# Optimization experiments

Hardware: AMD Instinct MI355X
Metric: run time of the kernel (lower is better)

## Reference

```python
import jax, jax.numpy as jnp
import numpy as np

B, S, H = 2, 2048, 2048
NK, NV, DK, DV = 16, 32, 128, 128
K_CONV = 4
EPS = 1e-6
KEY_DIM = NK * DK          # 2048
VALUE_DIM = NV * DV        # 4096
CONV_DIM = 2 * KEY_DIM + VALUE_DIM  # 8192
R = NV // NK               # GQA repeat factor


def setup_inputs() -> dict:
    key = jax.random.key(0)
    ks = jax.random.split(key, 9)
    s = lambda d: 1.0 / np.sqrt(d)
    x = jax.random.normal(ks[0], (B, S, H), jnp.float32)
    W_qkvz = jax.random.normal(ks[1], (H, 2 * KEY_DIM + 2 * VALUE_DIM), jnp.float32) * s(H)
    W_ba = jax.random.normal(ks[2], (H, 2 * NV), jnp.float32) * s(H)
    conv_w = jax.random.normal(ks[3], (CONV_DIM, K_CONV), jnp.float32) * s(K_CONV)
    dt_bias = jnp.ones((NV,), jnp.float32)
    A_log = jnp.log(jax.random.uniform(ks[4], (NV,), jnp.float32, 1e-3, 16.0))
    norm_w = jnp.ones((DV,), jnp.float32)
    W_out = jax.random.normal(ks[5], (VALUE_DIM, H), jnp.float32) * s(VALUE_DIM)
    return {"x": x, "W_qkvz": W_qkvz, "W_ba": W_ba, "conv_w": conv_w,
            "dt_bias": dt_bias, "A_log": A_log, "norm_w": norm_w, "W_out": W_out}


def _rms_norm(x, eps=EPS):
    return x * jax.lax.rsqrt(jnp.mean(jnp.square(x), -1, keepdims=True) + eps)


def _forward(x, W_qkvz, W_ba, conv_w, dt_bias, A_log, norm_w, W_out):
    b_, s_ = x.shape[:2]
    # in projections (mlx split-INDEX semantics)
    qkvz = (x @ W_qkvz).reshape(b_, s_, NK, 2 * DK + 2 * R * DV)
    q, k, v, z = jnp.split(qkvz, [DK, 2 * DK, 2 * DK + R * DV], axis=-1)
    v = v.reshape(b_, s_, NV, DV)
    z = z.reshape(b_, s_, NV, DV)
    ba = (x @ W_ba).reshape(b_, s_, NK, 2 * R)
    b_gate, a_gate = jnp.split(ba, [R], axis=-1)
    b_gate = b_gate.reshape(b_, s_, NV)
    a_gate = a_gate.reshape(b_, s_, NV)

    # causal depthwise conv over [q,k,v] channels, zero initial conv state
    mixed = jnp.concatenate([q.reshape(b_, s_, -1), k.reshape(b_, s_, -1),
                             v.reshape(b_, s_, -1)], axis=-1)  # [B,S,CONV_DIM]
    xc = jnp.pad(mixed, ((0, 0), (K_CONV - 1, 0), (0, 0))).transpose(0, 2, 1)  # [B,C,S+K-1]
    conv = jax.lax.conv_general_dilated(
        xc, conv_w[:, None, :], window_strides=(1,), padding='VALID',
        dimension_numbers=('NCH', 'OIH', 'NCH'), feature_group_count=CONV_DIM)
    conv = jax.nn.silu(conv).transpose(0, 2, 1)  # [B,S,CONV_DIM]
    q, k, v = jnp.split(conv, [KEY_DIM, 2 * KEY_DIM], axis=-1)
    q = q.reshape(b_, s_, NK, DK)
    k = k.reshape(b_, s_, NK, DK)
    v = v.reshape(b_, s_, NV, DV)

    inv_scale = DK ** -0.5
    q = (inv_scale ** 2) * _rms_norm(q)
    k = inv_scale * _rms_norm(k)
    # GQA: repeat k/q heads to match value heads
    q = jnp.repeat(q, R, axis=2)  # [B,S,NV,DK]
    k = jnp.repeat(k, R, axis=2)

    beta = jax.nn.sigmoid(b_gate)                                # [B,S,NV]
    g = -jnp.exp(A_log) * jax.nn.softplus(a_gate + dt_bias)      # [B,S,NV] (log-decay)

    # gated delta-rule recurrence, scan over time
    def step(Sst, inp):
        q_t, k_t, v_t, g_t, beta_t = inp   # [B,NV,DK], [B,NV,DV], [B,NV]
        Sst = Sst * jnp.exp(g_t)[..., None, None]
        kv = jnp.einsum('bhk,bhkv->bhv', k_t, Sst)
        delta = (v_t - kv) * beta_t[..., None]
        Sst = Sst + k_t[..., None] * delta[:, :, None, :]
        o = jnp.einsum('bhk,bhkv->bhv', q_t, Sst)
        return Sst, o

    S0 = jnp.zeros((b_, NV, DK, DV), x.dtype)
    xs = (q.transpose(1, 0, 2, 3), k.transpose(1, 0, 2, 3), v.transpose(1, 0, 2, 3),
          g.transpose(1, 0, 2), beta.transpose(1, 0, 2))
    _, out = jax.lax.scan(step, S0, xs)
    out = out.transpose(1, 0, 2, 3)  # [B,S,NV,DV]

    # gated RMSNorm (precise swiglu)
    xn = _rms_norm(out) * norm_w
    gated = jax.nn.silu(z.astype(jnp.float32)) * xn.astype(jnp.float32)
    gated = gated.astype(x.dtype)
    return gated.reshape(b_, s_, VALUE_DIM) @ W_out


def reference(x, W_qkvz, W_ba, conv_w, dt_bias, A_log, norm_w, W_out):
    return _forward(x, W_qkvz, W_ba, conv_w, dt_bias, A_log, norm_w, W_out)
```

## Files before the change

### kernel.cpp

```cpp
#include <hip/hip_runtime.h>
#include <stdint.h>

#define B_    2
#define SEQ   2048
#define HID   2048
#define NK_   16
#define NV_   32
#define DK_   128
#define DV_   128
#define NQKVZ 12288
#define CONVD 8192
#define MTOT  (B_*SEQ)
#define CCH   16
#define T0TOK 1264
#define HTOK2 784
#define CT    8
#define RLDSZ 110592

typedef unsigned short ushort_t;
typedef __bf16 bf16x8 __attribute__((ext_vector_type(8)));
typedef float  f32x4  __attribute__((ext_vector_type(4)));
typedef unsigned short us4 __attribute__((ext_vector_type(4)));

__device__ __forceinline__ ushort_t f2bf(float f){
  union { float f; unsigned u; } v; v.f = f;
  unsigned r = v.u + 0x7FFFu + ((v.u >> 16) & 1u);
  return (ushort_t)(r >> 16);
}
__device__ __forceinline__ float bf2f(ushort_t u){
  union { unsigned u; float f; } v; v.u = ((unsigned)u) << 16; return v.f;
}
__device__ __forceinline__ float sigmoidf_(float x){ return 1.f/(1.f+__expf(-x)); }
__device__ __forceinline__ float siluf_(float x){ return x*sigmoidf_(x); }

__global__ void cast_x_kernel(const float* __restrict__ x, ushort_t* __restrict__ xb, int n4){
  int i = blockIdx.x*256 + threadIdx.x;
  if (i >= n4) return;
  float4 v = ((const float4*)x)[i];
  us4 o; o[0]=f2bf(v.x); o[1]=f2bf(v.y); o[2]=f2bf(v.z); o[3]=f2bf(v.w);
  ((us4*)xb)[i] = o;
}

__global__ __launch_bounds__(256) void transpose_cast(const float* __restrict__ W, ushort_t* __restrict__ Wt,
                                                      int K, int N){
  __shared__ float tile[64][65];
  int n0 = blockIdx.x*64, k0 = blockIdx.y*64;
  int tx = threadIdx.x & 63, ty = threadIdx.x >> 6;
  #pragma unroll
  for (int i=0;i<16;i++){
    int kr = ty + i*4;
    tile[kr][tx] = W[(size_t)(k0+kr)*N + n0+tx];
  }
  __syncthreads();
  #pragma unroll
  for (int i=0;i<16;i++){
    int nr = ty + i*4;
    Wt[(size_t)(n0+nr)*K + k0+tx] = f2bf(tile[tx][nr]);
  }
}

template<int OUTBF>
__global__ __launch_bounds__(512, 2) void gemm_big(const ushort_t* __restrict__ A, const ushort_t* __restrict__ Bt,
                                                   void* __restrict__ Cv, int M, int N, int K){
  extern __shared__ ushort_t dynlds[];
  ushort_t* SA = dynlds;
  ushort_t* SB = dynlds + 3*8192;
  const int t = threadIdx.x;
  const int lane = t & 63, w = t >> 6;
  const int wm = w >> 2, wn = w & 3;
  const int lr = lane & 15, hk = lane >> 4;
  const int gx = gridDim.x;
  const int nwg = gx * gridDim.y;
  const int flat = blockIdx.y*gx + blockIdx.x;
  const int cpx = nwg >> 3;
  const int swzb = (flat & 7)*cpx + (flat >> 3);
  const int m0 = (swzb / gx) * 256, n0 = (swzb % gx) * 256;

  int srow[2], scol[2];
  #pragma unroll
  for (int q=0;q<2;q++){
    int p  = (w*2+q)*1024 + lane*16;
    int lg = p ^ (((p>>9)&1)<<5);
    srow[q] = lg >> 6;
    scol[q] = (lg & 63) >> 1;
  }
  int phA[8], phB[4];
  #pragma unroll
  for (int mi=0;mi<8;mi++){
    int lg = (wm*128 + mi*16 + lr)*64 + hk*16;
    phA[mi] = lg ^ (((lg>>9)&1)<<5);
  }
  #pragma unroll
  for (int ni=0;ni<4;ni++){
    int lg = (wn*64 + ni*16 + lr)*64 + hk*16;
    phB[ni] = lg ^ (((lg>>9)&1)<<5);
  }

  auto stage = [&](int j, int bufb){
    #pragma unroll
    for (int q=0;q<2;q++)
      __builtin_amdgcn_global_load_lds(
        (const __attribute__((address_space(1))) void*)(A + (size_t)(m0+srow[q])*K + j*32 + scol[q]),
        (__attribute__((address_space(3))) void*)(SA + bufb*8192 + (w*2+q)*512), 16, 0, 0);
    #pragma unroll
    for (int q=0;q<2;q++)
      __builtin_amdgcn_global_load_lds(
        (const __attribute__((address_space(1))) void*)(Bt + (size_t)(n0+srow[q])*K + j*32 + scol[q]),
        (__attribute__((address_space(3))) void*)(SB + bufb*8192 + (w*2+q)*512), 16, 0, 0);
  };

  f32x4 acc[8][4];
  #pragma unroll
  for (int mi=0;mi<8;mi++)
    #pragma unroll
    for (int ni=0;ni<4;ni++) acc[mi][ni] = (f32x4){0.f,0.f,0.f,0.f};

  const int NT = K >> 5;
  stage(0, 0);
  stage(1, 1);
  asm volatile("s_waitcnt vmcnt(4)" ::: "memory");
  __builtin_amdgcn_s_barrier();
  __builtin_amdgcn_sched_barrier(0);

  int cur = 0;
  for (int j = 0; j < NT; ++j){
    int nb = cur + 2; if (nb >= 3) nb -= 3;
    if (j + 2 < NT) stage(j+2, nb);
    const char* bA = (const char*)(SA + cur*8192);
    const char* bB = (const char*)(SB + cur*8192);
    bf16x8 af[8], bfv[4];
    #pragma unroll
    for (int mi=0;mi<8;mi++) af[mi]  = *(const bf16x8*)(bA + phA[mi]);
    #pragma unroll
    for (int ni=0;ni<4;ni++) bfv[ni] = *(const bf16x8*)(bB + phB[ni]);
    #pragma unroll
    for (int mi=0;mi<8;mi++)
      #pragma unroll
      for (int ni=0;ni<4;ni++)
        acc[mi][ni] = __builtin_amdgcn_mfma_f32_16x16x32_bf16(af[mi], bfv[ni], acc[mi][ni], 0, 0, 0);
    if (j + 2 < NT){
      asm volatile("s_waitcnt vmcnt(4)" ::: "memory");
      __builtin_amdgcn_s_barrier();
      __builtin_amdgcn_sched_barrier(0);
    } else if (j + 1 < NT){
      asm volatile("s_waitcnt vmcnt(0)" ::: "memory");
      __builtin_amdgcn_s_barrier();
      __builtin_amdgcn_sched_barrier(0);
    }
    cur = cur + 1; if (cur >= 3) cur -= 3;
  }

  #pragma unroll
  for (int mi=0;mi<8;mi++)
    #pragma unroll
    for (int ni=0;ni<4;ni++)
      #pragma unroll
      for (int r=0;r<4;r++){
        int m = m0 + wm*128 + mi*16 + hk*4 + r;
        int n = n0 + wn*64  + ni*16 + lr;
        if (OUTBF) ((ushort_t*)Cv)[(size_t)m*N + n] = f2bf(acc[mi][ni][r]);
        else       ((float*)Cv)[(size_t)m*N + n]    = acc[mi][ni][r];
      }
}

template<int OUTBF>
__global__ __launch_bounds__(512, 2) void gemm_big2(const ushort_t* __restrict__ A, const ushort_t* __restrict__ Bt,
                                                    void* __restrict__ Cv, int M, int N, int K){
  extern __shared__ ushort_t dynlds[];
  ushort_t* SA = dynlds;
  ushort_t* SB = dynlds + 3*8192;
  const int t = threadIdx.x;
  const int lane = t & 63, w = t >> 6;
  const int wm = w >> 1, wn = w & 1;
  const int lr = lane & 15, hk = lane >> 4;
  const int gx = gridDim.x;
  const int nwg = gx * gridDim.y;
  const int flat = blockIdx.y*gx + blockIdx.x;
  const int cpx = nwg >> 3;
  const int swzb = (flat & 7)*cpx + (flat >> 3);
  const int m0 = (swzb / gx) * 256, n0 = (swzb % gx) * 128;

  int srA[2], scA[2];
  #pragma unroll
  for (int q=0;q<2;q++){
    int p  = (w*2+q)*1024 + lane*16;
    int lg = p ^ (((p>>9)&1)<<5);
    srA[q] = lg >> 6;
    scA[q] = (lg & 63) >> 1;
  }
  int srB, scB;
  {
    int p  = w*1024 + lane*16;
    int lg = p ^ (((p>>9)&1)<<5);
    srB = lg >> 6;
    scB = (lg & 63) >> 1;
  }
  int phA[4], phB[4];
  #pragma unroll
  for (int mi=0;mi<4;mi++){
    int lg = (wm*64 + mi*16 + lr)*64 + hk*16;
    phA[mi] = lg ^ (((lg>>9)&1)<<5);
  }
  #pragma unroll
  for (int ni=0;ni<4;ni++){
    int lg = (wn*64 + ni*16 + lr)*64 + hk*16;
    phB[ni] = lg ^ (((lg>>9)&1)<<5);
  }

  auto stage = [&](int j, int bufb){
    #pragma unroll
    for (int q=0;q<2;q++)
      __builtin_amdgcn_global_load_lds(
        (const __attribute__((address_space(1))) void*)(A + (size_t)(m0+srA[q])*K + j*32 + scA[q]),
        (__attribute__((address_space(3))) void*)(SA + bufb*8192 + (w*2+q)*512), 16, 0, 0);
    __builtin_amdgcn_global_load_lds(
        (const __attribute__((address_space(1))) void*)(Bt + (size_t)(n0+srB)*K + j*32 + scB),
        (__attribute__((address_space(3))) void*)(SB + bufb*4096 + w*512), 16, 0, 0);
  };

  f32x4 acc[4][4];
  #pragma unroll
  for (int mi=0;mi<4;mi++)
    #pragma unroll
    for (int ni=0;ni<4;ni++) acc[mi][ni] = (f32x4){0.f,0.f,0.f,0.f};

  const int NT = K >> 5;
  stage(0, 0);
  stage(1, 1);
  asm volatile("s_waitcnt vmcnt(3)" ::: "memory");
  __builtin_amdgcn_s_barrier();
  __builtin_amdgcn_sched_barrier(0);

  int cur = 0;
  for (int j = 0; j < NT; ++j){
    int nb = cur + 2; if (nb >= 3) nb -= 3;
    if (j + 2 < NT) stage(j+2, nb);
    const char* bA = (const char*)(SA + cur*8192);
    const char* bB = (const char*)(SB + cur*4096);
    bf16x8 af[4], bfv[4];
    #pragma unroll
    for (int mi=0;mi<4;mi++) af[mi]  = *(const bf16x8*)(bA + phA[mi]);
    #pragma unroll
    for (int ni=0;ni<4;ni++) bfv[ni] = *(const bf16x8*)(bB + phB[ni]);
    #pragma unroll
    for (int mi=0;mi<4;mi++)
      #pragma unroll
      for (int ni=0;ni<4;ni++)
        acc[mi][ni] = __builtin_amdgcn_mfma_f32_16x16x32_bf16(af[mi], bfv[ni], acc[mi][ni], 0, 0, 0);
    if (j + 2 < NT){
      asm volatile("s_waitcnt vmcnt(3)" ::: "memory");
      __builtin_amdgcn_s_barrier();
      __builtin_amdgcn_sched_barrier(0);
    } else if (j + 1 < NT){
      asm volatile("s_waitcnt vmcnt(0)" ::: "memory");
      __builtin_amdgcn_s_barrier();
      __builtin_amdgcn_sched_barrier(0);
    }
    cur = cur + 1; if (cur >= 3) cur -= 3;
  }

  #pragma unroll
  for (int mi=0;mi<4;mi++)
    #pragma unroll
    for (int ni=0;ni<4;ni++)
      #pragma unroll
      for (int r=0;r<4;r++){
        int m = m0 + wm*64 + mi*16 + hk*4 + r;
        int n = n0 + wn*64 + ni*16 + lr;
        if (OUTBF) ((ushort_t*)Cv)[(size_t)m*N + n] = f2bf(acc[mi][ni][r]);
        else       ((float*)Cv)[(size_t)m*N + n]    = acc[mi][ni][r];
      }
}

__global__ __launch_bounds__(256) void gemm_ba(const float* __restrict__ x, const float* __restrict__ Wba,
                                               float* __restrict__ ba){
  int lane = threadIdx.x & 63;
  int wid  = threadIdx.x >> 6;
  int row  = blockIdx.x*4 + wid;
  const float* xr = x + (size_t)row*HID;
  float acc = 0.f;
  for (int k=0;k<HID;k+=4){
    float4 xv = *(const float4*)&xr[k];
    acc += xv.x * Wba[(size_t)(k+0)*64 + lane];
    acc += xv.y * Wba[(size_t)(k+1)*64 + lane];
    acc += xv.z * Wba[(size_t)(k+2)*64 + lane];
    acc += xv.w * Wba[(size_t)(k+3)*64 + lane];
  }
  ba[(size_t)row*64 + lane] = acc;
}

__global__ __launch_bounds__(256) void conv_norm_kernel(const ushort_t* __restrict__ qkvz, const float* __restrict__ conv_w,
                                                        ushort_t* __restrict__ qkv){
  const int blk = blockIdx.x;
  const int bt0 = (blk >> 4) * CT;
  const int ts0 = bt0 & (SEQ-1);
  const int gi = (blk & 15)*4 + (threadIdx.x >> 6);
  const int e2 = threadIdx.x & 63;
  const int dk = 2*e2;
  int col;
  if (gi < 16)       col = gi*768 + dk;
  else if (gi < 32)  col = (gi-16)*768 + 128 + dk;
  else { int nv = gi-32; col = (nv>>1)*768 + 256 + (nv&1)*128 + dk; }
  const int c = gi*128 + dk;
  const float4 w0 = *(const float4*)&conv_w[(size_t)c*4];
  const float4 w1 = *(const float4*)&conv_w[(size_t)(c+1)*4];
  ushort2 h0 = (ts0>=1) ? *(const ushort2*)&qkvz[(size_t)(bt0-3)*NQKVZ + col] : make_ushort2(0,0);
  ushort2 h1 = (ts0>=1) ? *(const ushort2*)&qkvz[(size_t)(bt0-2)*NQKVZ + col] : make_ushort2(0,0);
  ushort2 h2 = (ts0>=1) ? *(const ushort2*)&qkvz[(size_t)(bt0-1)*NQKVZ + col] : make_ushort2(0,0);
  const float scale = (gi < 16) ? (1.f/128.f) : 0.08838834764831845f;
  #pragma unroll
  for (int tt=0; tt<CT; ++tt){
    const int bt = bt0 + tt;
    ushort2 h3 = *(const ushort2*)&qkvz[(size_t)bt*NQKVZ + col];
    float y0 = siluf_(bf2f(h0.x)*w0.x + bf2f(h1.x)*w0.y + bf2f(h2.x)*w0.z + bf2f(h3.x)*w0.w);
    float y1 = siluf_(bf2f(h0.y)*w1.x + bf2f(h1.y)*w1.y + bf2f(h2.y)*w1.z + bf2f(h3.y)*w1.w);
    float o0 = y0, o1 = y1;
    if (gi < 32){
      float ss = y0*y0 + y1*y1;
      #pragma unroll
      for (int o=1;o<64;o<<=1) ss += __shfl_xor(ss, o);
      float rs = rsqrtf(ss*(1.f/128.f) + 1e-6f);
      o0 = y0*rs*scale; o1 = y1*rs*scale;
    }
    ushort2 ov; ov.x = f2bf(o0); ov.y = f2bf(o1);
    *(ushort2*)&qkv[(size_t)bt*CONVD + gi*128 + dk] = ov;
    h0 = h1; h1 = h2; h2 = h3;
  }
}

__global__ void gbeta_kernel(const float* __restrict__ ba, const float* __restrict__ A_log,
                             const float* __restrict__ dt_bias, float2* __restrict__ egb){
  int idx = blockIdx.x*256 + threadIdx.x;
  if (idx >= MTOT*NV_) return;
  int nv = idx & 31;
  int bt = idx >> 5;
  int nk = nv >> 1, r = nv & 1;
  float bg = ba[(size_t)bt*64 + nk*4 + r];
  float ag = ba[(size_t)bt*64 + nk*4 + 2 + r];
  float ad = ag + dt_bias[nv];
  float sp = fmaxf(ad, 0.f) + log1pf(__expf(-fabsf(ad)));
  float g  = -__expf(A_log[nv]) * sp;
  egb[idx] = make_float2(g, sigmoidf_(bg));
}

__global__ __launch_bounds__(512) void recurrence_chunked(const ushort_t* __restrict__ qkv,
                                                          const float2* __restrict__ egb,
                                                          float* __restrict__ outc,
                                                          ushort_t* __restrict__ oaug,
                                                          ushort_t* __restrict__ Sfin,
                                                          int pmode){
  extern __shared__ char rlds[];
  ushort_t* Kl  = (ushort_t*)(rlds + 0);
  ushort_t* S0h = (ushort_t*)(rlds + 4352);
  ushort_t* S0l = (ushort_t*)(rlds + 21760);
  ushort_t* T0h = (ushort_t*)(rlds + 39168);
  ushort_t* T0l = (ushort_t*)(rlds + 56576);
  ushort_t* KT  = (ushort_t*)(rlds + 73984);
  ushort_t* DT  = (ushort_t*)(rlds + 84224);
  ushort_t* Wl  = (ushort_t*)(rlds + 94464);
  float*    Al  = (float*)   (rlds + 95744);
  float*    Ul  = (float*)   (rlds + 97024);
  float*    clB = (float*)   (rlds + 107264);
  float*    blB = clB + 32;
  float*    eclB= clB + 64;
  float*    kslB= clB + 96;
  float*    c15B= clB + 128;

  const int bi = blockIdx.x;
  int hb, tokbase, ntok;
  bool ismrg = false, wsf = false;
  if (pmode == 0){ hb = bi; tokbase = 0; ntok = SEQ; }
  else {
    if (bi < 128){ hb = bi; tokbase = 0; ntok = T0TOK; wsf = true; }
    else { hb = bi - 128; tokbase = T0TOK; ntok = HTOK2; ismrg = true; }
  }
  const int b    = hb >> 6;
  const int nv   = (hb >> 1) & 31;
  const int half = hb & 1;
  const int nk   = nv >> 1;
  const int t    = threadIdx.x;
  const int lane = t & 63, w = t >> 6;
  const int lr   = lane & 15, hk = lane >> 4;

  for (int i = t; i < 128*40; i += 512){ KT[i] = 0; DT[i] = 0; }
  for (int i = t; i < 16*40;  i += 512) Wl[i] = 0;
  for (int i = t; i < 64*136; i += 512){
    S0h[i] = 0; S0l[i] = 0;
    if (ismrg){ T0h[i] = 0; T0l[i] = 0; }
  }
  __syncthreads();
  if (ismrg && t < 64) T0h[t*136 + half*64 + t] = (ushort_t)0x3F80;

  const int dt  = w >> 1;
  const int dkb = (w & 1) * 4;
  const int ot  = w - 4;
  const int st  = t >> 5, sdk = (t & 31) * 4;
  const size_t bt0 = (size_t)b*SEQ + tokbase;
  const int mytile = (w < 4) ? w : (w - 4);

  f32x4 S[4], T[4];
  #pragma unroll
  for (int tt=0;tt<4;tt++)
    #pragma unroll
    for (int r=0;r<4;r++){
      S[tt][r] = 0.f;
      T[tt][r] = (ismrg && ((dkb+tt)*16 + hk*4 + r) == (half*64 + dt*16 + lr)) ? 1.f : 0.f;
    }

  uint2 kreg = *(const uint2*)(qkv + (bt0+st)*CONVD + 2048 + nk*128 + sdk);
  bf16x8 qf[4];
  if (w >= 4){
    const ushort_t* qrow = qkv + (bt0+lr)*CONVD + nk*128 + hk*8;
    #pragma unroll
    for (int ks=0;ks<4;ks++) qf[ks] = *(const bf16x8*)(qrow + ks*32);
  }
  ushort_t vreg[4] = {0,0,0,0};
  if (w < 4){
    #pragma unroll
    for (int r=0;r<4;r++)
      vreg[r] = qkv[(bt0+hk*4+r)*CONVD + 4096 + nv*128 + half*64 + w*16 + lr];
  }
  {
    float2 gb = make_float2(0.f,0.f);
    if (w==1 && lane<16) gb = egb[(bt0+lane)*NV_ + nv];
    *(uint2*)&Kl[st*136 + sdk] = kreg;
    if (w==1 && lane<16){
      float c = gb.x;
      #pragma unroll
      for (int o=1;o<16;o<<=1){ float tv = __shfl_up(c, o, 16); if (lane >= o) c += tv; }
      clB[lane] = c; blB[lane] = gb.y; eclB[lane] = __expf(c);
      float c15 = __shfl(c, 15, 16);
      kslB[lane] = __expf(c15 - c);
      if (lane==0) c15B[0] = c15;
    }
  }
  __syncthreads();

  int pb = 0;
  for (int base = 0; base < ntok; base += CCH){
    const int nbase = (base + CCH < ntok) ? base + CCH : base;
    const int pb16 = pb*16;

    bf16x8 kf[4];
    if (w <= 4){
      #pragma unroll
      for (int ks=0;ks<4;ks++) kf[ks] = *(const bf16x8*)&Kl[lr*136 + hk*8 + ks*32];
    }
    f32x4 ph = (f32x4){0.f,0.f,0.f,0.f}, pl = ph, phA = ph, plA = ph;
    __builtin_amdgcn_s_setprio(1);
    #pragma unroll
    for (int ks=0;ks<4;ks++){
      bf16x8 xf = (w < 4) ? kf[ks] : qf[ks];
      bf16x8 yh = *(const bf16x8*)&S0h[(mytile*16+lr)*136 + hk*8 + ks*32];
      bf16x8 yl = *(const bf16x8*)&S0l[(mytile*16+lr)*136 + hk*8 + ks*32];
      ph = __builtin_amdgcn_mfma_f32_16x16x32_bf16(xf, yh, ph, 0,0,0);
      pl = __builtin_amdgcn_mfma_f32_16x16x32_bf16(xf, yl, pl, 0,0,0);
    }
    if (ismrg){
      #pragma unroll
      for (int ks=0;ks<4;ks++){
        bf16x8 xf = (w < 4) ? kf[ks] : qf[ks];
        bf16x8 yh = *(const bf16x8*)&T0h[(mytile*16+lr)*136 + hk*8 + ks*32];
        bf16x8 yl = *(const bf16x8*)&T0l[(mytile*16+lr)*136 + hk*8 + ks*32];
        phA = __builtin_amdgcn_mfma_f32_16x16x32_bf16(xf, yh, phA, 0,0,0);
        plA = __builtin_amdgcn_mfma_f32_16x16x32_bf16(xf, yl, plA, 0,0,0);
      }
    }
    __builtin_amdgcn_s_setprio(0);
    if (w == 1){
      f32x4 a = (f32x4){0.f,0.f,0.f,0.f};
      #pragma unroll
      for (int ks=0;ks<4;ks++) a = __builtin_amdgcn_mfma_f32_16x16x32_bf16(kf[ks], kf[ks], a, 0,0,0);
      #pragma unroll
      for (int r=0;r<4;r++){
        int i = hk*4 + r, j = lr;
        Al[i*20 + j] = (j < i) ? blB[pb16+i]*__expf(clB[pb16+i]-clB[pb16+j])*a[r] : 0.f;
      }
    }
    if (w == 4){
      f32x4 a = (f32x4){0.f,0.f,0.f,0.f};
      #pragma unroll
      for (int ks=0;ks<4;ks++) a = __builtin_amdgcn_mfma_f32_16x16x32_bf16(qf[ks], kf[ks], a, 0,0,0);
      #pragma unroll
      for (int r=0;r<4;r++){
        int i = hk*4 + r, j = lr;
        float val = (j <= i) ? __expf(clB[pb16+i]-clB[pb16+j])*a[r] : 0.f;
        Wl[i*40 + j] = f2bf(val);
      }
    }
    if (w < 4){
      float4 uu;
      #pragma unroll
      for (int r=0;r<4;r++){
        int i = hk*4 + r;
        ((float*)&uu)[r] = blB[pb16+i]*(bf2f(vreg[r]) - eclB[pb16+i]*(ph[r] + pl[r]));
      }
      *(float4*)&Ul[(w*16 + lr)*20 + hk*4] = uu;
      if (ismrg){
        float4 ua;
        #pragma unroll
        for (int r=0;r<4;r++){
          int i = hk*4 + r;
          ((float*)&ua)[r] = -blB[pb16+i]*eclB[pb16+i]*(phA[r] + plA[r]);
        }
        *(float4*)&Ul[(64 + w*16 + lr)*20 + hk*4] = ua;
      }
    }
    if (w == 2 || w == 3){
      int dk = t & 127;
      #pragma unroll
      for (int j=0;j<16;j+=2){
        unsigned p0 = f2bf(kslB[pb16+j]  * bf2f(Kl[j*136     + dk]));
        unsigned p1 = f2bf(kslB[pb16+j+1]* bf2f(Kl[(j+1)*136 + dk]));
        *(unsigned*)&KT[dk*40 + j] = p0 | (p1 << 16);
      }
    }
    __syncthreads();

    kreg = *(const uint2*)(qkv + (bt0+nbase+st)*CONVD + 2048 + nk*128 + sdk);
    if (w >= 4){
      const ushort_t* qrow = qkv + (bt0 + nbase + lr)*CONVD + nk*128 + hk*8;
      #pragma unroll
      for (int ks=0;ks<4;ks++) qf[ks] = *(const bf16x8*)(qrow + ks*32);
    }
    if (w < 4){
      #pragma unroll
      for (int r=0;r<4;r++)
        vreg[r] = qkv[(bt0+nbase+hk*4+r)*CONVD + 4096 + nv*128 + half*64 + w*16 + lr];
    }
    float2 ebn = make_float2(0.f,0.f);
    if (w==1 && lane<16) ebn = egb[(bt0+nbase+lane)*NV_ + nv];
    bf16x8 yf[4];
    #pragma unroll
    for (int tt=0;tt<4;tt++) yf[tt] = *(const bf16x8*)&KT[((dkb+tt)*16+lr)*40 + hk*8];
    bf16x8 wfr;
    if (w >= 4) wfr = *(const bf16x8*)&Wl[lr*40 + hk*8];

    auto fsub = [&](int rowoff){
      float d[16];
      #pragma unroll
      for (int q=0;q<4;q++){
        float4 dd = *(const float4*)&Ul[(rowoff+lane)*20 + q*4];
        d[4*q]=dd.x; d[4*q+1]=dd.y; d[4*q+2]=dd.z; d[4*q+3]=dd.w;
      }
      #pragma unroll
      for (int rb=0;rb<4;rb++){
        float p0=0.f,p1=0.f,p2=0.f,p3=0.f;
        #pragma unroll
        for (int jb=0;jb<rb;jb++){
          float4 A0 = *(const float4*)&Al[(rb*4+0)*20 + jb*4];
          float4 A1 = *(const float4*)&Al[(rb*4+1)*20 + jb*4];
          float4 A2 = *(const float4*)&Al[(rb*4+2)*20 + jb*4];
          float4 A3 = *(const float4*)&Al[(rb*4+3)*20 + jb*4];
          p0 += A0.x*d[jb*4]+A0.y*d[jb*4+1]+A0.z*d[jb*4+2]+A0.w*d[jb*4+3];
          p1 += A1.x*d[jb*4]+A1.y*d[jb*4+1]+A1.z*d[jb*4+2]+A1.w*d[jb*4+3];
          p2 += A2.x*d[jb*4]+A2.y*d[jb*4+1]+A2.z*d[jb*4+2]+A2.w*d[jb*4+3];
          p3 += A3.x*d[jb*4]+A3.y*d[jb*4+1]+A3.z*d[jb*4+2]+A3.w*d[jb*4+3];
        }
        const int r0 = rb*4;
        d[r0+0] -= p0;
        d[r0+1] -= p1 + Al[(r0+1)*20+r0]*d[r0];
        d[r0+2] -= p2 + Al[(r0+2)*20+r0]*d[r0] + Al[(r0+2)*20+r0+1]*d[r0+1];
        d[r0+3] -= p3 + Al[(r0+3)*20+r0]*d[r0] + Al[(r0+3)*20+r0+1]*d[r0+1] + Al[(r0+3)*20+r0+2]*d[r0+2];
      }
      unsigned dd[8];
      #pragma unroll
      for (int p=0;p<8;p++) dd[p] = (unsigned)f2bf(d[2*p]) | ((unsigned)f2bf(d[2*p+1]) << 16);
      *(uint4*)&DT[(rowoff+lane)*40 + 0] = make_uint4(dd[0],dd[1],dd[2],dd[3]);
      *(uint4*)&DT[(rowoff+lane)*40 + 8] = make_uint4(dd[4],dd[5],dd[6],dd[7]);
    };
    if (w == 0){ __builtin_amdgcn_s_setprio(1); fsub(0);  __builtin_amdgcn_s_setprio(0); }
    if (ismrg && w == 1){ __builtin_amdgcn_s_setprio(1); fsub(64); __builtin_amdgcn_s_setprio(0); }
    __syncthreads();

    if (w >= 4){
      bf16x8 dfr = *(const bf16x8*)&DT[(ot*16+lr)*40 + hk*8];
      f32x4 oo = __builtin_amdgcn_mfma_f32_16x16x32_bf16(wfr, dfr, (f32x4){0.f,0.f,0.f,0.f}, 0,0,0);
      #pragma unroll
      for (int r=0;r<4;r++){
        int i = hk*4 + r;
        outc[((bt0+base+i)*NV_ + nv)*(size_t)DV_ + half*64 + ot*16 + lr] = oo[r] + eclB[pb16+i]*(ph[r] + pl[r]);
      }
      if (ismrg){
        bf16x8 dfr2 = *(const bf16x8*)&DT[(64 + ot*16+lr)*40 + hk*8];
        f32x4 oo2 = __builtin_amdgcn_mfma_f32_16x16x32_bf16(wfr, dfr2, (f32x4){0.f,0.f,0.f,0.f}, 0,0,0);
        #pragma unroll
        for (int r=0;r<4;r++){
          int i = hk*4 + r;
          oaug[(((size_t)(b*NV_+nv))*HTOK2 + base + i)*128 + half*64 + ot*16 + lr]
            = f2bf(oo2[r] + eclB[pb16+i]*(phA[r] + plA[r]));
        }
      }
    }
    {
      float g15 = __expf(c15B[pb]);
      bf16x8 dB = *(const bf16x8*)&DT[(dt*16+lr)*40 + hk*8];
      __builtin_amdgcn_s_setprio(1);
      #pragma unroll
      for (int tt=0;tt<4;tt++){
        f32x4 s = S[tt];
        s[0]*=g15; s[1]*=g15; s[2]*=g15; s[3]*=g15;
        S[tt] = __builtin_amdgcn_mfma_f32_16x16x32_bf16(yf[tt], dB, s, 0,0,0);
      }
      if (ismrg){
        bf16x8 dB2 = *(const bf16x8*)&DT[(64 + dt*16+lr)*40 + hk*8];
        #pragma unroll
        for (int tt=0;tt<4;tt++){
          f32x4 s = T[tt];
          s[0]*=g15; s[1]*=g15; s[2]*=g15; s[3]*=g15;
          T[tt] = __builtin_amdgcn_mfma_f32_16x16x32_bf16(yf[tt], dB2, s, 0,0,0);
        }
      }
      __builtin_amdgcn_s_setprio(0);
    }
    {
      const int dv = dt*16 + lr;
      #pragma unroll
      for (int tt=0;tt<4;tt++){
        const int dk0 = (dkb+tt)*16 + hk*4;
        {
          float s0=S[tt][0], s1=S[tt][1], s2=S[tt][2], s3=S[tt][3];
          ushort_t h0=f2bf(s0), h1=f2bf(s1), h2=f2bf(s2), h3=f2bf(s3);
          *(uint2*)&S0h[dv*136 + dk0] = make_uint2((unsigned)h0 | ((unsigned)h1<<16),
                                                   (unsigned)h2 | ((unsigned)h3<<16));
          *(uint2*)&S0l[dv*136 + dk0] = make_uint2((unsigned)f2bf(s0-bf2f(h0)) | ((unsigned)f2bf(s1-bf2f(h1))<<16),
                                                   (unsigned)f2bf(s2-bf2f(h2)) | ((unsigned)f2bf(s3-bf2f(h3))<<16));
        }
        if (ismrg){
          float s0=T[tt][0], s1=T[tt][1], s2=T[tt][2], s3=T[tt][3];
          ushort_t h0=f2bf(s0), h1=f2bf(s1), h2=f2bf(s2), h3=f2bf(s3);
          *(uint2*)&T0h[dv*136 + dk0] = make_uint2((unsigned)h0 | ((unsigned)h1<<16),
                                                   (unsigned)h2 | ((unsigned)h3<<16));
          *(uint2*)&T0l[dv*136 + dk0] = make_uint2((unsigned)f2bf(s0-bf2f(h0)) | ((unsigned)f2bf(s1-bf2f(h1))<<16),
                                                   (unsigned)f2bf(s2-bf2f(h2)) | ((unsigned)f2bf(s3-bf2f(h3))<<16));
        }
      }
    }
    *(uint2*)&Kl[st*136 + sdk] = kreg;
    if (w==1 && lane<16){
      float c = ebn.x;
      #pragma unroll
      for (int o=1;o<16;o<<=1){ float tv = __shfl_up(c, o, 16); if (lane >= o) c += tv; }
      int q16 = (pb^1)*16;
      clB[q16+lane] = c; blB[q16+lane] = ebn.y; eclB[q16+lane] = __expf(c);
      float c15 = __shfl(c, 15, 16);
      kslB[q16+lane] = __expf(c15 - c);
      if (lane==0) c15B[pb^1] = c15;
    }
    __syncthreads();
    pb ^= 1;
  }

  if (wsf){
    for (int i = t; i < 64*128; i += 512){
      int dvl = i >> 7, dk = i & 127;
      size_t row = ((size_t)(b*NV_+nv)*128 + half*64 + dvl)*256;
      Sfin[row + dk]       = S0h[dvl*136 + dk];
      Sfin[row + 128 + dk] = S0l[dvl*136 + dk];
    }
  }
}

__global__ __launch_bounds__(256) void corr_gemm(const ushort_t* __restrict__ oaug, const ushort_t* __restrict__ Sfin,
                                                 float* __restrict__ core){
  __shared__ ushort_t As[128][32];
  __shared__ ushort_t Bs[128][32];
  const int head = blockIdx.y;
  const int m0 = blockIdx.x * 128;
  const int b = head >> 5, nv = head & 31;
  const int t = threadIdx.x, lane = t & 63, w = t >> 6;
  const int wm = w >> 1, wn = w & 1;
  const int srow = lane >> 2, scol = (lane & 3) * 8;
  const ushort_t* Abase = oaug + (size_t)head*HTOK2*128;
  const ushort_t* Bbase = Sfin + (size_t)head*128*256;
  ushort_t* lA0 = &As[     w*16][0];
  ushort_t* lA1 = &As[64 + w*16][0];
  ushort_t* lB0 = &Bs[     w*16][0];
  ushort_t* lB1 = &Bs[64 + w*16][0];
  f32x4 acc[4][4];
  #pragma unroll
  for (int i=0;i<4;i++)
    #pragma unroll
    for (int j=0;j<4;j++) acc[i][j] = (f32x4){0.f,0.f,0.f,0.f};
  const int lr = lane & 15, lk = (lane >> 4) * 8;
  for (int k0 = 0; k0 < 256; k0 += 32){
    const int ka = k0 & 127;
    int ra0 = m0 +      w*16 + srow; if (ra0 >= HTOK2) ra0 = HTOK2 - 1;
    int ra1 = m0 + 64 + w*16 + srow; if (ra1 >= HTOK2) ra1 = HTOK2 - 1;
    __builtin_amdgcn_global_load_lds((const __attribute__((address_space(1))) void*)(Abase + (size_t)ra0*128 + ka + scol),
                                     (__attribute__((address_space(3))) void*)lA0, 16, 0, 0);
    __builtin_amdgcn_global_load_lds((const __attribute__((address_space(1))) void*)(Abase + (size_t)ra1*128 + ka + scol),
                                     (__attribute__((address_space(3))) void*)lA1, 16, 0, 0);
    __builtin_amdgcn_global_load_lds((const __attribute__((address_space(1))) void*)(Bbase + (size_t)(     w*16 + srow)*256 + k0 + scol),
                                     (__attribute__((address_space(3))) void*)lB0, 16, 0, 0);
    __builtin_amdgcn_global_load_lds((const __attribute__((address_space(1))) void*)(Bbase + (size_t)(64 + w*16 + srow)*256 + k0 + scol),
                                     (__attribute__((address_space(3))) void*)lB1, 16, 0, 0);
    __syncthreads();
    bf16x8 af[4], bfv[4];
    #pragma unroll
    for (int i=0;i<4;i++) af[i]  = *(const bf16x8*)&As[wm*64 + i*16 + lr][lk];
    #pragma unroll
    for (int j=0;j<4;j++) bfv[j] = *(const bf16x8*)&Bs[wn*64 + j*16 + lr][lk];
    #pragma unroll
    for (int i=0;i<4;i++)
      #pragma unroll
      for (int j=0;j<4;j++)
        acc[i][j] = __builtin_amdgcn_mfma_f32_16x16x32_bf16(af[i], bfv[j], acc[i][j], 0, 0, 0);
    __syncthreads();
  }
  const int lg = lane >> 4;
  #pragma unroll
  for (int i=0;i<4;i++)
    #pragma unroll
    for (int j=0;j<4;j++)
      #pragma unroll
      for (int r=0;r<4;r++){
        int m = m0 + wm*64 + i*16 + lg*4 + r;
        int n = wn*64 + j*16 + lr;
        if (m < HTOK2){
          float* p = &core[(((size_t)b*SEQ + T0TOK + m)*NV_ + nv)*(size_t)DV_ + n];
          *p += acc[i][j][r];
        }
      }
}

__global__ __launch_bounds__(128) void gatenorm_kernel(const float* __restrict__ outc, const ushort_t* __restrict__ qkvz,
                                                       const float* __restrict__ norm_w, ushort_t* __restrict__ gated){
  __shared__ float red[2];
  const int blk = blockIdx.x;
  const int nv = blk & 31;
  const size_t bt = (size_t)(blk >> 5);
  const int dv = threadIdx.x;
  float xv = outc[(bt*NV_ + nv)*(size_t)DV_ + dv];
  float ss = xv*xv;
  #pragma unroll
  for (int o=1;o<64;o<<=1) ss += __shfl_xor(ss, o);
  if ((threadIdx.x & 63)==0) red[threadIdx.x>>6] = ss;
  __syncthreads();
  float tot = red[0]+red[1];
  float xn = xv * rsqrtf(tot*(1.f/128.f) + 1e-6f) * norm_w[dv];
  int nk = nv>>1, r = nv&1;
  float z = bf2f(qkvz[bt*NQKVZ + nk*768 + 512 + r*128 + dv]);
  gated[bt*(size_t)4096 + nv*128 + dv] = f2bf(siluf_(z)*xn);
}

extern "C" void kernel_launch(void* const* d_in, const int* in_sizes, int n_in,
                              void* d_out, int out_size, void* d_ws, size_t ws_size,
                              hipStream_t stream){
  (void)in_sizes; (void)n_in; (void)out_size;
  const float* x      = (const float*)d_in[0];
  const float* W_qkvz = (const float*)d_in[1];
  const float* W_ba   = (const float*)d_in[2];
  const float* conv_w = (const float*)d_in[3];
  const float* dt_bias= (const float*)d_in[4];
  const float* A_log  = (const float*)d_in[5];
  const float* norm_w = (const float*)d_in[6];
  const float* W_out  = (const float*)d_in[7];
  float* outp = (float*)d_out;

  char* w = (char*)d_ws;
  const size_t R0 = 0;
  const size_t R1 = 100663296;
  const size_t R2 = R1 + 67108864;
  const size_t R3 = R2 + 67108864;
  const size_t R4 = R3 + 2097152;
  const size_t NEED_SP = R4 + 16777216 + 4194304;
  ushort_t* qkvz_bf = (ushort_t*)(w + R0);
  ushort_t* xb      = (ushort_t*)(w + R1);
  ushort_t* wqt     = (ushort_t*)(w + R1 + 16777216);
  ushort_t* qkv_bf  = (ushort_t*)(w + R1);
  ushort_t* gated   = (ushort_t*)(w + R1);
  float*    core    = (float*)   (w + R2);
  ushort_t* wot     = (ushort_t*)(w + R2);
  float*    ba      = (float*)   (w + R3);
  float2*   egb     = (float2*)  (w + R3 + 1048576);
  ushort_t* oaug    = (ushort_t*)(w + R4);
  ushort_t* Sfin    = (ushort_t*)(w + R4 + 16777216);

  hipError_t e1 = hipFuncSetAttribute((const void*)gemm_big<1>, hipFuncAttributeMaxDynamicSharedMemorySize, 98304);
  hipError_t e2 = hipFuncSetAttribute((const void*)gemm_big2<0>, hipFuncAttributeMaxDynamicSharedMemorySize, 73728);
  hipError_t e3 = hipFuncSetAttribute((const void*)recurrence_chunked, hipFuncAttributeMaxDynamicSharedMemorySize, RLDSZ);
  (void)e1; (void)e2;
  const bool seqpar = (ws_size >= NEED_SP) && (e3 == hipSuccess);

  cast_x_kernel<<<(MTOT*HID/4 + 255)/256, 256, 0, stream>>>(x, xb, MTOT*HID/4);
  transpose_cast<<<dim3(NQKVZ/64, HID/64), 256, 0, stream>>>(W_qkvz, wqt, HID, NQKVZ);
  gemm_big<1><<<dim3(NQKVZ/256, MTOT/256), 512, 98304, stream>>>(xb, wqt, (void*)qkvz_bf, MTOT, NQKVZ, HID);
  gemm_ba<<<MTOT/4, 256, 0, stream>>>(x, W_ba, ba);
  gbeta_kernel<<<(MTOT*NV_+255)/256, 256, 0, stream>>>(ba, A_log, dt_bias, egb);
  conv_norm_kernel<<<(MTOT/CT)*16, 256, 0, stream>>>(qkvz_bf, conv_w, qkv_bf);
  if (seqpar){
    recurrence_chunked<<<256, 512, RLDSZ, stream>>>(qkv_bf, egb, core, oaug, Sfin, 1);
    corr_gemm<<<dim3((HTOK2 + 127)/128, 64), 256, 0, stream>>>(oaug, Sfin, core);
  } else {
    recurrence_chunked<<<128, 512, RLDSZ, stream>>>(qkv_bf, egb, core, oaug, Sfin, 0);
  }
  gatenorm_kernel<<<MTOT*NV_, 128, 0, stream>>>(core, qkvz_bf, norm_w, gated);
  transpose_cast<<<dim3(2048/64, 4096/64), 256, 0, stream>>>(W_out, wot, 4096, 2048);
  gemm_big2<0><<<dim3(2048/128, MTOT/256), 512, 73728, stream>>>(gated, wot, (void*)outp, MTOT, 2048, 4096);
}
```

Before: 853.1 us.

## Compute triangular-solve fragments redundantly in registers, drop DT staging and barrier

Instead of one or two waves solving the 16x16 lower-triangular system into an LDS buffer and then hitting a barrier, each wave solves the rows it needs in registers and packs them straight into MFMA B fragments. This removes the DT LDS round trip and one __syncthreads per chunk on the serial recurrence path. The cost is redundant forward-substitution work in every wave, which adds VALU work and register pressure. The token split between the two phases of the recurrence is also rebalanced.

After: 1.399 ms. 1.64x slower.

```diff
diff --git a/kernel.cpp b/kernel.cpp
--- a/kernel.cpp
+++ b/kernel.cpp
@@ -12,8 +12,8 @@
 #define CONVD 8192
 #define MTOT  (B_*SEQ)
 #define CCH   16
-#define T0TOK 1264
-#define HTOK2 784
+#define T0TOK 1216
+#define HTOK2 832
 #define CT    8
 #define RLDSZ 110592
 
@@ -356,7 +356,6 @@
   ushort_t* T0h = (ushort_t*)(rlds + 39168);
   ushort_t* T0l = (ushort_t*)(rlds + 56576);
   ushort_t* KT  = (ushort_t*)(rlds + 73984);
-  ushort_t* DT  = (ushort_t*)(rlds + 84224);
   ushort_t* Wl  = (ushort_t*)(rlds + 94464);
   float*    Al  = (float*)   (rlds + 95744);
   float*    Ul  = (float*)   (rlds + 97024);
@@ -382,7 +381,7 @@
   const int lane = t & 63, w = t >> 6;
   const int lr   = lane & 15, hk = lane >> 4;
 
-  for (int i = t; i < 128*40; i += 512){ KT[i] = 0; DT[i] = 0; }
+  for (int i = t; i < 128*40; i += 512) KT[i] = 0;
   for (int i = t; i < 16*40;  i += 512) Wl[i] = 0;
   for (int i = t; i < 64*136; i += 512){
     S0h[i] = 0; S0l[i] = 0;
@@ -536,12 +535,12 @@
     bf16x8 wfr;
     if (w >= 4) wfr = *(const bf16x8*)&Wl[lr*40 + hk*8];
 
-    auto fsub = [&](int rowoff){
-      float d[16];
+    float dtmp[16];
+    auto fsub_reg = [&](int colrow){
       #pragma unroll
       for (int q=0;q<4;q++){
-        float4 dd = *(const float4*)&Ul[(rowoff+lane)*20 + q*4];
-        d[4*q]=dd.x; d[4*q+1]=dd.y; d[4*q+2]=dd.z; d[4*q+3]=dd.w;
+        float4 dd = *(const float4*)&Ul[colrow*20 + q*4];
+        dtmp[4*q]=dd.x; dtmp[4*q+1]=dd.y; dtmp[4*q+2]=dd.z; dtmp[4*q+3]=dd.w;
       }
       #pragma unroll
       for (int rb=0;rb<4;rb++){
@@ -552,38 +551,47 @@
           float4 A1 = *(const float4*)&Al[(rb*4+1)*20 + jb*4];
           float4 A2 = *(const float4*)&Al[(rb*4+2)*20 + jb*4];
           float4 A3 = *(const float4*)&Al[(rb*4+3)*20 + jb*4];
-          p0 += A0.x*d[jb*4]+A0.y*d[jb*4+1]+A0.z*d[jb*4+2]+A0.w*d[jb*4+3];
-          p1 += A1.x*d[jb*4]+A1.y*d[jb*4+1]+A1.z*d[jb*4+2]+A1.w*d[jb*4+3];
-          p2 += A2.x*d[jb*4]+A2.y*d[jb*4+1]+A2.z*d[jb*4+2]+A2.w*d[jb*4+3];
-          p3 += A3.x*d[jb*4]+A3.y*d[jb*4+1]+A3.z*d[jb*4+2]+A3.w*d[jb*4+3];
+          p0 += A0.x*dtmp[jb*4]+A0.y*dtmp[jb*4+1]+A0.z*dtmp[jb*4+2]+A0.w*dtmp[jb*4+3];
+          p1 += A1.x*dtmp[jb*4]+A1.y*dtmp[jb*4+1]+A1.z*dtmp[jb*4+2]+A1.w*dtmp[jb*4+3];
+          p2 += A2.x*dtmp[jb*4]+A2.y*dtmp[jb*4+1]+A2.z*dtmp[jb*4+2]+A2.w*dtmp[jb*4+3];
+          p3 += A3.x*dtmp[jb*4]+A3.y*dtmp[jb*4+1]+A3.z*dtmp[jb*4+2]+A3.w*dtmp[jb*4+3];
         }
         const int r0 = rb*4;
-        d[r0+0] -= p0;
-        d[r0+1] -= p1 + Al[(r0+1)*20+r0]*d[r0];
-        d[r0+2] -= p2 + Al[(r0+2)*20+r0]*d[r0] + Al[(r0+2)*20+r0+1]*d[r0+1];
-        d[r0+3] -= p3 + Al[(r0+3)*20+r0]*d[r0] + Al[(r0+3)*20+r0+1]*d[r0+1] + Al[(r0+3)*20+r0+2]*d[r0+2];
-      }
-      unsigned dd[8];
-      #pragma unroll
-      for (int p=0;p<8;p++) dd[p] = (unsigned)f2bf(d[2*p]) | ((unsigned)f2bf(d[2*p+1]) << 16);
-      *(uint4*)&DT[(rowoff+lane)*40 + 0] = make_uint4(dd[0],dd[1],dd[2],dd[3]);
-      *(uint4*)&DT[(rowoff+lane)*40 + 8] = make_uint4(dd[4],dd[5],dd[6],dd[7]);
+        dtmp[r0+0] -= p0;
+        dtmp[r0+1] -= p1 + Al[(r0+1)*20+r0]*dtmp[r0];
+        dtmp[r0+2] -= p2 + Al[(r0+2)*20+r0]*dtmp[r0] + Al[(r0+2)*20+r0+1]*dtmp[r0+1];
+        dtmp[r0+3] -= p3 + Al[(r0+3)*20+r0]*dtmp[r0] + Al[(r0+3)*20+r0+1]*dtmp[r0+1] + Al[(r0+3)*20+r0+2]*dtmp[r0+2];
+      }
     };
-    if (w == 0){ __builtin_amdgcn_s_setprio(1); fsub(0);  __builtin_amdgcn_s_setprio(0); }
-    if (ismrg && w == 1){ __builtin_amdgcn_s_setprio(1); fsub(64); __builtin_amdgcn_s_setprio(0); }
-    __syncthreads();
+    auto mkfrag = [&]()->bf16x8{
+      union { bf16x8 v; ushort_t u[8]; } r;
+      #pragma unroll
+      for (int j=0;j<8;j++)
+        r.u[j] = (hk < 2) ? f2bf(dtmp[(hk*8 + j) & 15]) : (ushort_t)0;
+      return r.v;
+    };
+
+    __builtin_amdgcn_s_setprio(1);
+    fsub_reg(dt*16 + lr);
+    bf16x8 fB = mkfrag();
+    bf16x8 fO = {};
+    if (w >= 4){ fsub_reg(ot*16 + lr); fO = mkfrag(); }
+    bf16x8 fBA = {}, fOA = {};
+    if (ismrg){
+      fsub_reg(64 + dt*16 + lr); fBA = mkfrag();
+      if (w >= 4){ fsub_reg(64 + ot*16 + lr); fOA = mkfrag(); }
+    }
+    __builtin_amdgcn_s_setprio(0);
 
     if (w >= 4){
-      bf16x8 dfr = *(const bf16x8*)&DT[(ot*16+lr)*40 + hk*8];
-      f32x4 oo = __builtin_amdgcn_mfma_f32_16x16x32_bf16(wfr, dfr, (f32x4){0.f,0.f,0.f,0.f}, 0,0,0);
+      f32x4 oo = __builtin_amdgcn_mfma_f32_16x16x32_bf16(wfr, fO, (f32x4){0.f,0.f,0.f,0.f}, 0,0,0);
       #pragma unroll
       for (int r=0;r<4;r++){
         int i = hk*4 + r;
         outc[((bt0+base+i)*NV_ + nv)*(size_t)DV_ + half*64 + ot*16 + lr] = oo[r] + eclB[pb16+i]*(ph[r] + pl[r]);
       }
       if (ismrg){
-        bf16x8 dfr2 = *(const bf16x8*)&DT[(64 + ot*16+lr)*40 + hk*8];
-        f32x4 oo2 = __builtin_amdgcn_mfma_f32_16x16x32_bf16(wfr, dfr2, (f32x4){0.f,0.f,0.f,0.f}, 0,0,0);
+        f32x4 oo2 = __builtin_amdgcn_mfma_f32_16x16x32_bf16(wfr, fOA, (f32x4){0.f,0.f,0.f,0.f}, 0,0,0);
         #pragma unroll
         for (int r=0;r<4;r++){
           int i = hk*4 + r;
@@ -594,21 +602,19 @@
     }
     {
       float g15 = __expf(c15B[pb]);
-      bf16x8 dB = *(const bf16x8*)&DT[(dt*16+lr)*40 + hk*8];
       __builtin_amdgcn_s_setprio(1);
       #pragma unroll
       for (int tt=0;tt<4;tt++){
         f32x4 s = S[tt];
         s[0]*=g15; s[1]*=g15; s[2]*=g15; s[3]*=g15;
-        S[tt] = __builtin_amdgcn_mfma_f32_16x16x32_bf16(yf[tt], dB, s, 0,0,0);
+        S[tt] = __builtin_amdgcn_mfma_f32_16x16x32_bf16(yf[tt], fB, s, 0,0,0);
       }
       if (ismrg){
-        bf16x8 dB2 = *(const bf16x8*)&DT[(64 + dt*16+lr)*40 + hk*8];
         #pragma unroll
         for (int tt=0;tt<4;tt++){
           f32x4 s = T[tt];
           s[0]*=g15; s[1]*=g15; s[2]*=g15; s[3]*=g15;
-          T[tt] = __builtin_amdgcn_mfma_f32_16x16x32_bf16(yf[tt], dB2, s, 0,0,0);
+          T[tt] = __builtin_amdgcn_mfma_f32_16x16x32_bf16(yf[tt], fBA, s, 0,0,0);
         }
       }
       __builtin_amdgcn_s_setprio(0);
```
